# Kernel optimization log

Hardware: AMD Instinct MI355X
Metric: run time of the kernel (lower is better)

Reference implementation:

```python
import jax, jax.numpy as jnp
import numpy as np

DIM = 512
NUM_HEADS = 8
HEAD_DIM = DIM // NUM_HEADS
FFN_DIM = 4 * DIM
EPS = 1e-6


def rmsnorm(x, w):
    rms = jnp.sqrt(jnp.mean(x * x, axis=-1, keepdims=True) + EPS)
    return x / rms * w


def setup_inputs() -> dict:
    key = jax.random.key(0)
    ks = jax.random.split(key, 8)
    B, T = 4, 2048
    x = jax.random.normal(ks[0], (B, T, DIM), dtype=jnp.float32)
    # Linear weights stored as [in, out] (transpose of torch layout)
    w_qkv = jax.random.normal(ks[1], (DIM, 3 * DIM), dtype=jnp.float32) * 0.02
    w_out = jax.random.normal(ks[2], (DIM, DIM), dtype=jnp.float32) * 0.02
    b_out = jnp.zeros((DIM,), dtype=jnp.float32)
    w1 = jax.random.normal(ks[3], (DIM, FFN_DIM), dtype=jnp.float32) * 0.02
    b1 = jnp.zeros((FFN_DIM,), dtype=jnp.float32)
    w2 = jax.random.normal(ks[4], (FFN_DIM, DIM), dtype=jnp.float32) * 0.02
    b2 = jnp.zeros((DIM,), dtype=jnp.float32)
    norm1_w = jnp.ones((DIM,), dtype=jnp.float32)
    norm2_w = jnp.ones((DIM,), dtype=jnp.float32)
    return {
        "x": x, "norm1_w": norm1_w, "norm2_w": norm2_w,
        "w_qkv": w_qkv, "w_out": w_out, "b_out": b_out,
        "w1": w1, "b1": b1, "w2": w2, "b2": b2,
        "context_size": 64,
    }


def reference(x, norm1_w, norm2_w, w_qkv, w_out, b_out, w1, b1, w2, b2, context_size):
    B, T, D = x.shape
    H, Hd = NUM_HEADS, HEAD_DIM
    # --- attention sublayer ---
    xn = rmsnorm(x, norm1_w)
    qkv = xn @ w_qkv                      # (B, T, 3D)
    q, k, v = jnp.split(qkv, 3, axis=-1)
    q = q.reshape(B, T, H, Hd).transpose(0, 2, 1, 3)  # (B, H, T, Hd)
    k = k.reshape(B, T, H, Hd).transpose(0, 2, 1, 3)
    v = v.reshape(B, T, H, Hd).transpose(0, 2, 1, 3)
    scale = Hd ** -0.5
    scores = jnp.einsum('bhqd,bhkd->bhqk', q, k) * scale  # (B, H, T, T)
    idx = jnp.arange(T)
    band = jnp.abs(idx[:, None] - idx[None, :]) <= context_size  # (T, T)
    scores = jnp.where(band[None, None], scores, -jnp.inf)
    attn = jax.nn.softmax(scores, axis=-1)
    out = jnp.einsum('bhqk,bhkd->bhqd', attn, v)  # (B, H, T, Hd)
    out = out.transpose(0, 2, 1, 3).reshape(B, T, D)
    out = out @ w_out + b_out
    x = x + out
    # --- FFN sublayer ---
    h = rmsnorm(x, norm2_w)
    h = jax.nn.gelu(h @ w1 + b1, approximate=False)
    x = x + (h @ w2 + b2)
    return x
```

## Files before the change

kernel.cpp:

```cpp
#include <hip/hip_runtime.h>
#include <cstdint>
#include <cstddef>

#define B_  4
#define T_  2048
#define D_  512
#define NH_ 8
#define HD_ 64
#define FF_ 2048
#define M_  (B_*T_)

typedef unsigned short u16;
typedef __attribute__((ext_vector_type(8))) unsigned short u16x8;
typedef __attribute__((ext_vector_type(8))) __bf16         bf16x8;
typedef __attribute__((ext_vector_type(4))) float          f32x4;

__device__ __forceinline__ u16 f2bf(float f) {
  unsigned u = __float_as_uint(f);
  u += 0x7FFF + ((u >> 16) & 1);
  return (u16)(u >> 16);
}

__device__ __forceinline__ f32x4 mfma_bf16(u16x8 a, u16x8 b, f32x4 c) {
  return __builtin_amdgcn_mfma_f32_16x16x32_bf16(
      __builtin_bit_cast(bf16x8, a), __builtin_bit_cast(bf16x8, b), c, 0, 0, 0);
}

__device__ __forceinline__ void async16(const void* g, void* l) {
  __builtin_amdgcn_global_load_lds(
      (const __attribute__((address_space(1))) unsigned int*)g,
      (__attribute__((address_space(3))) unsigned int*)l, 16, 0, 0);
}

__global__ __launch_bounds__(256) void trans_kernel(const float* __restrict__ in,
                                                    u16* __restrict__ out,
                                                    int R, int C) {
  __shared__ float tile[32][33];
  int c0 = blockIdx.x * 32, r0 = blockIdx.y * 32;
  int tx = threadIdx.x, ty = threadIdx.y;
#pragma unroll
  for (int i = 0; i < 4; i++)
    tile[ty + i * 8][tx] = in[(size_t)(r0 + ty + i * 8) * C + c0 + tx];
  __syncthreads();
#pragma unroll
  for (int i = 0; i < 4; i++)
    out[(size_t)(c0 + ty + i * 8) * R + r0 + tx] = f2bf(tile[tx][ty + i * 8]);
}

__global__ __launch_bounds__(256) void rmsnorm_kernel(const float* __restrict__ x,
                                                      const float* __restrict__ w,
                                                      u16* __restrict__ out) {
  int row  = blockIdx.x * 4 + (threadIdx.x >> 6);
  int lane = threadIdx.x & 63;
  const float* xr = x + (size_t)row * D_ + lane * 8;
  float4 v0 = *(const float4*)xr;
  float4 v1 = *(const float4*)(xr + 4);
  float ss = v0.x*v0.x + v0.y*v0.y + v0.z*v0.z + v0.w*v0.w
           + v1.x*v1.x + v1.y*v1.y + v1.z*v1.z + v1.w*v1.w;
#pragma unroll
  for (int m = 1; m < 64; m <<= 1) ss += __shfl_xor(ss, m, 64);
  float inv = rsqrtf(ss * (1.0f / D_) + 1e-6f);
  const float* wr = w + lane * 8;
  float4 w0 = *(const float4*)wr;
  float4 w1v = *(const float4*)(wr + 4);
  u16 o[8];
  o[0] = f2bf(v0.x * inv * w0.x);  o[1] = f2bf(v0.y * inv * w0.y);
  o[2] = f2bf(v0.z * inv * w0.z);  o[3] = f2bf(v0.w * inv * w0.w);
  o[4] = f2bf(v1.x * inv * w1v.x); o[5] = f2bf(v1.y * inv * w1v.y);
  o[6] = f2bf(v1.z * inv * w1v.z); o[7] = f2bf(v1.w * inv * w1v.w);
  *(uint4*)(out + (size_t)row * D_ + lane * 8) = *(uint4*)o;
}

template <int BN, bool HAS_BIAS, bool HAS_RES, bool DO_GELU, bool STORE_BF16>
__global__ __launch_bounds__(256) void gemm_kernel(
    const u16* __restrict__ A, const u16* __restrict__ Bt, void* __restrict__ Cv,
    const float* __restrict__ bias, const float* __restrict__ res,
    int M, int N, int K) {
  constexpr int BCH = BN / 32;
  constexpr int NJ  = BN / 32;
  constexpr int EW  = BN + 4;
  __shared__ __align__(16) char smem[16384 + BN * 128];
  u16* ldsA = (u16*)smem;
  u16* ldsB = (u16*)(smem + 16384);
  const int tid = threadIdx.x;
  const int lane = tid & 63, w = tid >> 6;
  const int quad = lane >> 4, m16 = lane & 15;
  const int wm = w & 1, wn = w >> 1;
  const int m0 = blockIdx.y * 128, n0 = blockIdx.x * BN;

  f32x4 acc[4][NJ];
#pragma unroll
  for (int i = 0; i < 4; i++)
#pragma unroll
    for (int j = 0; j < NJ; j++) acc[i][j] = (f32x4){0.f, 0.f, 0.f, 0.f};

  const int srow = tid >> 3;
  const int scol = (((tid & 7) ^ (srow & 7))) * 8;
  const u16* Ag = A  + (size_t)(m0 + srow) * K + scol;
  const u16* Bg = Bt + (size_t)(n0 + srow) * K + scol;

  for (int kt = 0; kt < K; kt += 64) {
#pragma unroll
    for (int c = 0; c < 4; c++)
      async16(Ag + (size_t)c * 32 * K + kt, smem + c * 4096 + tid * 16);
#pragma unroll
    for (int c = 0; c < BCH; c++)
      async16(Bg + (size_t)c * 32 * K + kt, smem + 16384 + c * 4096 + tid * 16);
    __syncthreads();
#pragma unroll
    for (int kk = 0; kk < 2; kk++) {
      const int sl = ((kk * 4 + quad) ^ (m16 & 7)) * 8;
      const u16* pa = ldsA + (wm * 64 + m16) * 64 + sl;
      const u16* pb = ldsB + (wn * (BN / 2) + m16) * 64 + sl;
      u16x8 af[4], bfr[NJ];
#pragma unroll
      for (int i = 0; i < 4; i++) af[i] = *(const u16x8*)(pa + i * 1024);
#pragma unroll
      for (int j = 0; j < NJ; j++) bfr[j] = *(const u16x8*)(pb + j * 1024);
#pragma unroll
      for (int i = 0; i < 4; i++)
#pragma unroll
        for (int j = 0; j < NJ; j++)
          acc[i][j] = mfma_bf16(af[i], bfr[j], acc[i][j]);
    }
    __syncthreads();
  }

  float* eps = (float*)smem;
#pragma unroll
  for (int i = 0; i < 4; i++) {
    __syncthreads();
#pragma unroll
    for (int j = 0; j < NJ; j++)
#pragma unroll
      for (int r = 0; r < 4; r++)
        eps[(wm * 16 + quad * 4 + r) * EW + wn * (BN / 2) + j * 16 + m16] =
            acc[i][j][r];
    __syncthreads();
    constexpr int REPS = (32 * BN) / (256 * 8);
#pragma unroll
    for (int rep = 0; rep < REPS; rep++) {
      const int lr  = (BN == 128) ? (rep * 16 + (tid >> 4)) : (tid >> 3);
      const int col = (BN == 128) ? ((tid & 15) * 8) : ((tid & 7) * 8);
      const int rg  = m0 + (lr >> 4) * 64 + i * 16 + (lr & 15);
      float v[8];
      *(float4*)(v)     = *(const float4*)(eps + lr * EW + col);
      *(float4*)(v + 4) = *(const float4*)(eps + lr * EW + col + 4);
      if (HAS_BIAS) {
        float4 b0 = *(const float4*)(bias + n0 + col);
        float4 b1 = *(const float4*)(bias + n0 + col + 4);
        v[0] += b0.x; v[1] += b0.y; v[2] += b0.z; v[3] += b0.w;
        v[4] += b1.x; v[5] += b1.y; v[6] += b1.z; v[7] += b1.w;
      }
      if (DO_GELU) {
#pragma unroll
        for (int e = 0; e < 8; e++)
          v[e] = 0.5f * v[e] * (1.0f + erff(v[e] * 0.70710678118f));
      }
      const size_t idx = (size_t)rg * N + n0 + col;
      if (HAS_RES) {
        float4 r0 = *(const float4*)(res + idx);
        float4 r1 = *(const float4*)(res + idx + 4);
        v[0] += r0.x; v[1] += r0.y; v[2] += r0.z; v[3] += r0.w;
        v[4] += r1.x; v[5] += r1.y; v[6] += r1.z; v[7] += r1.w;
      }
      if (STORE_BF16) {
        u16 o[8];
#pragma unroll
        for (int e = 0; e < 8; e++) o[e] = f2bf(v[e]);
        *(uint4*)((u16*)Cv + idx) = *(uint4*)o;
      } else {
        *(float4*)((float*)Cv + idx)     = *(float4*)(v);
        *(float4*)((float*)Cv + idx + 4) = *(float4*)(v + 4);
      }
    }
  }
}

#define KP_ 72
__global__ __launch_bounds__(256) void attn_kernel(const u16* __restrict__ qkv,
                                                   u16* __restrict__ out) {
  __shared__ __align__(16) char smem[57600];
  u16* Ks = (u16*)smem;
  u16* Vt = (u16*)(smem + 29952);
  const int tid = threadIdx.x, lane = tid & 63, w = tid >> 6;
  const int quad = lane >> 4, m16 = lane & 15;
  const int q0 = blockIdx.x * 64, h = blockIdx.y, b = blockIdx.z;
  const int kstart = q0 - 64;
  const u16* base = qkv + (size_t)b * T_ * 1536;

  for (int c = tid; c < 1664; c += 256) {
    int row = c >> 3, cc = (c & 7) * 8;
    int j = kstart + row;
    j = j < 0 ? 0 : (j > T_ - 1 ? T_ - 1 : j);
    *(uint4*)(Ks + row * KP_ + cc) =
        *(const uint4*)(base + (size_t)j * 1536 + 512 + h * 64 + cc);
  }
  for (int c = tid; c < 1664; c += 256) {
    int row = c >> 3, cc = (c & 7) * 8;
    int j = kstart + row;
    j = j < 0 ? 0 : (j > T_ - 1 ? T_ - 1 : j);
    uint4 u = *(const uint4*)(base + (size_t)j * 1536 + 1024 + h * 64 + cc);
    u16 tmp[8];
    *(uint4*)tmp = u;
#pragma unroll
    for (int i = 0; i < 8; i++) Vt[(cc + i) * 216 + row] = tmp[i];
  }
  const int qw = q0 + w * 16;
  const u16* qb = base + (size_t)(qw + m16) * 1536 + h * 64 + quad * 8;
  u16x8 a0 = *(const u16x8*)qb;
  u16x8 a1 = *(const u16x8*)(qb + 32);
  __syncthreads();

  float s[10][4];
#pragma unroll
  for (int t = 0; t < 10; t++) {
    int kt = (w + t) * 16;
    u16x8 kb0 = *(const u16x8*)(Ks + (kt + m16) * KP_ + quad * 8);
    u16x8 kb1 = *(const u16x8*)(Ks + (kt + m16) * KP_ + 32 + quad * 8);
    f32x4 acc = {0.f, 0.f, 0.f, 0.f};
    acc = mfma_bf16(a0, kb0, acc);
    acc = mfma_bf16(a1, kb1, acc);
    int jab = kstart + kt + m16;
#pragma unroll
    for (int r = 0; r < 4; r++) {
      int q = qw + quad * 4 + r;
      int d = q - jab;
      bool valid = (jab >= 0) && (jab < T_) && (d <= 64) && (d >= -64);
      s[t][r] = valid ? acc[r] * 0.125f : -1e30f;
    }
  }
  float mx[4], sm[4];
#pragma unroll
  for (int r = 0; r < 4; r++) mx[r] = -1e30f;
#pragma unroll
  for (int t = 0; t < 10; t++)
#pragma unroll
    for (int r = 0; r < 4; r++) mx[r] = fmaxf(mx[r], s[t][r]);
#pragma unroll
  for (int r = 0; r < 4; r++) {
#pragma unroll
    for (int msk = 1; msk < 16; msk <<= 1)
      mx[r] = fmaxf(mx[r], __shfl_xor(mx[r], msk, 64));
    sm[r] = 0.f;
  }
#pragma unroll
  for (int t = 0; t < 10; t++)
#pragma unroll
    for (int r = 0; r < 4; r++) {
      float e = __expf(s[t][r] - mx[r]);
      s[t][r] = e; sm[r] += e;
    }
#pragma unroll
  for (int r = 0; r < 4; r++) {
#pragma unroll
    for (int msk = 1; msk < 16; msk <<= 1) sm[r] += __shfl_xor(sm[r], msk, 64);
    sm[r] = 1.0f / sm[r];
  }
  __syncthreads();
  u16* Ps = (u16*)smem + w * 2688;
#pragma unroll
  for (int t = 0; t < 10; t++)
#pragma unroll
    for (int r = 0; r < 4; r++)
      Ps[(quad * 4 + r) * 168 + t * 16 + m16] = f2bf(s[t][r] * sm[r]);
  __syncthreads();

  f32x4 o[4];
#pragma unroll
  for (int dt = 0; dt < 4; dt++) o[dt] = (f32x4){0.f, 0.f, 0.f, 0.f};
#pragma unroll
  for (int c5 = 0; c5 < 5; c5++) {
    u16x8 pa = *(const u16x8*)(Ps + m16 * 168 + c5 * 32 + quad * 8);
#pragma unroll
    for (int dt = 0; dt < 4; dt++) {
      u16x8 vb = *(const u16x8*)(Vt + (dt * 16 + m16) * 216 + w * 16 + c5 * 32 + quad * 8);
      o[dt] = mfma_bf16(pa, vb, o[dt]);
    }
  }
#pragma unroll
  for (int dt = 0; dt < 4; dt++)
#pragma unroll
    for (int r = 0; r < 4; r++)
      out[(size_t)(b * T_ + qw + quad * 4 + r) * D_ + h * HD_ + dt * 16 + m16] =
          f2bf(o[dt][r]);
}

extern "C" void kernel_launch(void* const* d_in, const int* in_sizes, int n_in,
                              void* d_out, int out_size, void* d_ws, size_t ws_size,
                              hipStream_t stream) {
  (void)in_sizes; (void)n_in; (void)out_size; (void)ws_size;
  const float* x     = (const float*)d_in[0];
  const float* n1w   = (const float*)d_in[1];
  const float* n2w   = (const float*)d_in[2];
  const float* w_qkv = (const float*)d_in[3];
  const float* w_out = (const float*)d_in[4];
  const float* b_out = (const float*)d_in[5];
  const float* w1    = (const float*)d_in[6];
  const float* b1    = (const float*)d_in[7];
  const float* w2    = (const float*)d_in[8];
  const float* b2    = (const float*)d_in[9];
  float* out = (float*)d_out;
  char* ws = (char*)d_ws;

  u16* wqkvT  = (u16*)(ws + 0);
  u16* woutT  = (u16*)(ws + 1572864);
  u16* w1T    = (u16*)(ws + 2097152);
  u16* w2T    = (u16*)(ws + 4194304);
  u16* xn     = (u16*)(ws + 6291456);
  u16* qkv    = (u16*)(ws + 14680064);
  u16* attno  = (u16*)(ws + 39845888);
  float* x1   = (float*)(ws + 48234496);
  u16* hn     = xn;
  u16* hbuf   = qkv;

  dim3 tb(32, 8);
  trans_kernel<<<dim3(48, 16), tb, 0, stream>>>(w_qkv, wqkvT, 512, 1536);
  trans_kernel<<<dim3(16, 16), tb, 0, stream>>>(w_out, woutT, 512, 512);
  trans_kernel<<<dim3(64, 16), tb, 0, stream>>>(w1,   w1T,   512, 2048);
  trans_kernel<<<dim3(16, 64), tb, 0, stream>>>(w2,   w2T,   2048, 512);

  rmsnorm_kernel<<<2048, 256, 0, stream>>>(x, n1w, xn);
  gemm_kernel<128, false, false, false, true><<<dim3(12, 64), 256, 0, stream>>>(
      xn, wqkvT, (void*)qkv, nullptr, nullptr, M_, 3 * D_, D_);
  attn_kernel<<<dim3(32, 8, 4), 256, 0, stream>>>(qkv, attno);
  gemm_kernel<64, true, true, false, false><<<dim3(8, 64), 256, 0, stream>>>(
      attno, woutT, (void*)x1, b_out, x, M_, D_, D_);
  rmsnorm_kernel<<<2048, 256, 0, stream>>>(x1, n2w, hn);
  gemm_kernel<128, true, false, true, true><<<dim3(16, 64), 256, 0, stream>>>(
      hn, w1T, (void*)hbuf, b1, nullptr, M_, FF_, D_);
  gemm_kernel<64, true, true, false, false><<<dim3(8, 64), 256, 0, stream>>>(
      hbuf, w2T, (void*)out, b2, x1, M_, D_, FF_);
}
```

Baseline: 244.8 us.

## Merge weight transposes, add BM tiling, fast GELU, pad V tile

Fuses the four weight-transpose launches into one kernel, and makes the GEMM block-M size a template parameter so the N=512 GEMMs run 64x64 tiles over twice as many blocks. It also hoists the bias loads out of the epilogue loop and replaces erff in GELU with an Abramowitz-Stegun polynomial using a fast reciprocal and exp. Separately, it changes the transposed-V LDS row pitch from 216 to 218 to reduce bank conflicts. The GELU approximation has roughly 1e-7 absolute error and may use an approximate reciprocal.

```diff
diff --git a/kernel.cpp b/kernel.cpp
--- a/kernel.cpp
+++ b/kernel.cpp
@@ -32,11 +32,34 @@
       (__attribute__((address_space(3))) unsigned int*)l, 16, 0, 0);
 }
 
-__global__ __launch_bounds__(256) void trans_kernel(const float* __restrict__ in,
-                                                    u16* __restrict__ out,
-                                                    int R, int C) {
+__device__ __forceinline__ float gelu_f(float v) {
+  float ax = fabsf(v) * 0.70710678118f;
+#if __has_builtin(__builtin_amdgcn_rcpf)
+  float t = __builtin_amdgcn_rcpf(1.0f + 0.3275911f * ax);
+#else
+  float t = 1.0f / (1.0f + 0.3275911f * ax);
+#endif
+  float p = ((((1.061405429f * t - 1.453152027f) * t + 1.421413741f) * t
+              - 0.284496736f) * t + 0.254829592f) * t;
+  float e = __expf(-ax * ax);
+  float er = 1.0f - p * e;
+  float s = (v >= 0.0f) ? er : -er;
+  return 0.5f * v * (1.0f + s);
+}
+
+__global__ __launch_bounds__(256) void trans4_kernel(
+    const float* __restrict__ i0, u16* __restrict__ o0,
+    const float* __restrict__ i1, u16* __restrict__ o1,
+    const float* __restrict__ i2, u16* __restrict__ o2,
+    const float* __restrict__ i3, u16* __restrict__ o3) {
   __shared__ float tile[32][33];
-  int c0 = blockIdx.x * 32, r0 = blockIdx.y * 32;
+  int bid = blockIdx.x;
+  const float* in; u16* out; int R, C, gx, lb;
+  if (bid < 768)       { in = i0; out = o0; R = 512;  C = 1536; gx = 48; lb = bid; }
+  else if (bid < 1024) { in = i1; out = o1; R = 512;  C = 512;  gx = 16; lb = bid - 768; }
+  else if (bid < 2048) { in = i2; out = o2; R = 512;  C = 2048; gx = 64; lb = bid - 1024; }
+  else                 { in = i3; out = o3; R = 2048; C = 512;  gx = 16; lb = bid - 2048; }
+  int c0 = (lb % gx) * 32, r0 = (lb / gx) * 32;
   int tx = threadIdx.x, ty = threadIdx.y;
 #pragma unroll
   for (int i = 0; i < 4; i++)
@@ -71,26 +94,28 @@
   *(uint4*)(out + (size_t)row * D_ + lane * 8) = *(uint4*)o;
 }
 
-template <int BN, bool HAS_BIAS, bool HAS_RES, bool DO_GELU, bool STORE_BF16>
+template <int BM, int BN, bool HAS_BIAS, bool HAS_RES, bool DO_GELU, bool STORE_BF16>
 __global__ __launch_bounds__(256) void gemm_kernel(
     const u16* __restrict__ A, const u16* __restrict__ Bt, void* __restrict__ Cv,
     const float* __restrict__ bias, const float* __restrict__ res,
     int M, int N, int K) {
+  constexpr int ACH = BM / 32;
   constexpr int BCH = BN / 32;
-  constexpr int NJ  = BN / 32;
+  constexpr int WM  = BM / 2, WN = BN / 2;
+  constexpr int MI  = WM / 16, NJ = WN / 16;
   constexpr int EW  = BN + 4;
-  __shared__ __align__(16) char smem[16384 + BN * 128];
+  __shared__ __align__(16) char smem[BM * 128 + BN * 128];
   u16* ldsA = (u16*)smem;
-  u16* ldsB = (u16*)(smem + 16384);
+  u16* ldsB = (u16*)(smem + BM * 128);
   const int tid = threadIdx.x;
   const int lane = tid & 63, w = tid >> 6;
   const int quad = lane >> 4, m16 = lane & 15;
   const int wm = w & 1, wn = w >> 1;
-  const int m0 = blockIdx.y * 128, n0 = blockIdx.x * BN;
-
-  f32x4 acc[4][NJ];
-#pragma unroll
-  for (int i = 0; i < 4; i++)
+  const int m0 = blockIdx.y * BM, n0 = blockIdx.x * BN;
+
+  f32x4 acc[MI][NJ];
+#pragma unroll
+  for (int i = 0; i < MI; i++)
 #pragma unroll
     for (int j = 0; j < NJ; j++) acc[i][j] = (f32x4){0.f, 0.f, 0.f, 0.f};
 
@@ -101,24 +126,24 @@
 
   for (int kt = 0; kt < K; kt += 64) {
 #pragma unroll
-    for (int c = 0; c < 4; c++)
+    for (int c = 0; c < ACH; c++)
       async16(Ag + (size_t)c * 32 * K + kt, smem + c * 4096 + tid * 16);
 #pragma unroll
     for (int c = 0; c < BCH; c++)
-      async16(Bg + (size_t)c * 32 * K + kt, smem + 16384 + c * 4096 + tid * 16);
+      async16(Bg + (size_t)c * 32 * K + kt, smem + BM * 128 + c * 4096 + tid * 16);
     __syncthreads();
 #pragma unroll
     for (int kk = 0; kk < 2; kk++) {
       const int sl = ((kk * 4 + quad) ^ (m16 & 7)) * 8;
-      const u16* pa = ldsA + (wm * 64 + m16) * 64 + sl;
-      const u16* pb = ldsB + (wn * (BN / 2) + m16) * 64 + sl;
-      u16x8 af[4], bfr[NJ];
-#pragma unroll
-      for (int i = 0; i < 4; i++) af[i] = *(const u16x8*)(pa + i * 1024);
+      const u16* pa = ldsA + (wm * WM + m16) * 64 + sl;
+      const u16* pb = ldsB + (wn * WN + m16) * 64 + sl;
+      u16x8 af[MI], bfr[NJ];
+#pragma unroll
+      for (int i = 0; i < MI; i++) af[i] = *(const u16x8*)(pa + i * 1024);
 #pragma unroll
       for (int j = 0; j < NJ; j++) bfr[j] = *(const u16x8*)(pb + j * 1024);
 #pragma unroll
-      for (int i = 0; i < 4; i++)
+      for (int i = 0; i < MI; i++)
 #pragma unroll
         for (int j = 0; j < NJ; j++)
           acc[i][j] = mfma_bf16(af[i], bfr[j], acc[i][j]);
@@ -127,35 +152,41 @@
   }
 
   float* eps = (float*)smem;
-#pragma unroll
-  for (int i = 0; i < 4; i++) {
+  constexpr int REPS = (32 * BN) / (256 * 8);
+  float bv[REPS][8];
+  if (HAS_BIAS) {
+#pragma unroll
+    for (int rep = 0; rep < REPS; rep++) {
+      const int col = (BN == 128) ? ((tid & 15) * 8) : ((tid & 7) * 8);
+      *(float4*)(bv[rep])     = *(const float4*)(bias + n0 + col);
+      *(float4*)(bv[rep] + 4) = *(const float4*)(bias + n0 + col + 4);
+    }
+  }
+#pragma unroll
+  for (int i = 0; i < MI; i++) {
     __syncthreads();
 #pragma unroll
     for (int j = 0; j < NJ; j++)
 #pragma unroll
       for (int r = 0; r < 4; r++)
-        eps[(wm * 16 + quad * 4 + r) * EW + wn * (BN / 2) + j * 16 + m16] =
+        eps[(wm * 16 + quad * 4 + r) * EW + wn * WN + j * 16 + m16] =
             acc[i][j][r];
     __syncthreads();
-    constexpr int REPS = (32 * BN) / (256 * 8);
 #pragma unroll
     for (int rep = 0; rep < REPS; rep++) {
       const int lr  = (BN == 128) ? (rep * 16 + (tid >> 4)) : (tid >> 3);
       const int col = (BN == 128) ? ((tid & 15) * 8) : ((tid & 7) * 8);
-      const int rg  = m0 + (lr >> 4) * 64 + i * 16 + (lr & 15);
+      const int rg  = m0 + (lr >> 4) * WM + i * 16 + (lr & 15);
       float v[8];
       *(float4*)(v)     = *(const float4*)(eps + lr * EW + col);
       *(float4*)(v + 4) = *(const float4*)(eps + lr * EW + col + 4);
       if (HAS_BIAS) {
-        float4 b0 = *(const float4*)(bias + n0 + col);
-        float4 b1 = *(const float4*)(bias + n0 + col + 4);
-        v[0] += b0.x; v[1] += b0.y; v[2] += b0.z; v[3] += b0.w;
-        v[4] += b1.x; v[5] += b1.y; v[6] += b1.z; v[7] += b1.w;
+#pragma unroll
+        for (int e = 0; e < 8; e++) v[e] += bv[rep][e];
       }
       if (DO_GELU) {
 #pragma unroll
-        for (int e = 0; e < 8; e++)
-          v[e] = 0.5f * v[e] * (1.0f + erff(v[e] * 0.70710678118f));
+        for (int e = 0; e < 8; e++) v[e] = gelu_f(v[e]);
       }
       const size_t idx = (size_t)rg * N + n0 + col;
       if (HAS_RES) {
@@ -178,9 +209,10 @@
 }
 
 #define KP_ 72
+#define VP_ 218
 __global__ __launch_bounds__(256) void attn_kernel(const u16* __restrict__ qkv,
                                                    u16* __restrict__ out) {
-  __shared__ __align__(16) char smem[57600];
+  __shared__ __align__(16) char smem[29952 + 64 * VP_ * 2];
   u16* Ks = (u16*)smem;
   u16* Vt = (u16*)(smem + 29952);
   const int tid = threadIdx.x, lane = tid & 63, w = tid >> 6;
@@ -204,7 +236,7 @@
     u16 tmp[8];
     *(uint4*)tmp = u;
 #pragma unroll
-    for (int i = 0; i < 8; i++) Vt[(cc + i) * 216 + row] = tmp[i];
+    for (int i = 0; i < 8; i++) Vt[(cc + i) * VP_ + row] = tmp[i];
   }
   const int qw = q0 + w * 16;
   const u16* qb = base + (size_t)(qw + m16) * 1536 + h * 64 + quad * 8;
@@ -274,7 +306,7 @@
     u16x8 pa = *(const u16x8*)(Ps + m16 * 168 + c5 * 32 + quad * 8);
 #pragma unroll
     for (int dt = 0; dt < 4; dt++) {
-      u16x8 vb = *(const u16x8*)(Vt + (dt * 16 + m16) * 216 + w * 16 + c5 * 32 + quad * 8);
+      u16x8 vb = *(const u16x8*)(Vt + (dt * 16 + m16) * VP_ + w * 16 + c5 * 32 + quad * 8);
       o[dt] = mfma_bf16(pa, vb, o[dt]);
     }
   }
@@ -314,21 +346,18 @@
   u16* hn     = xn;
   u16* hbuf   = qkv;
 
-  dim3 tb(32, 8);
-  trans_kernel<<<dim3(48, 16), tb, 0, stream>>>(w_qkv, wqkvT, 512, 1536);
-  trans_kernel<<<dim3(16, 16), tb, 0, stream>>>(w_out, woutT, 512, 512);
-  trans_kernel<<<dim3(64, 16), tb, 0, stream>>>(w1,   w1T,   512, 2048);
-  trans_kernel<<<dim3(16, 64), tb, 0, stream>>>(w2,   w2T,   2048, 512);
+  trans4_kernel<<<3072, dim3(32, 8), 0, stream>>>(
+      w_qkv, wqkvT, w_out, woutT, w1, w1T, w2, w2T);
 
   rmsnorm_kernel<<<2048, 256, 0, stream>>>(x, n1w, xn);
-  gemm_kernel<128, false, false, false, true><<<dim3(12, 64), 256, 0, stream>>>(
+  gemm_kernel<128, 128, false, false, false, true><<<dim3(12, 64), 256, 0, stream>>>(
       xn, wqkvT, (void*)qkv, nullptr, nullptr, M_, 3 * D_, D_);
   attn_kernel<<<dim3(32, 8, 4), 256, 0, stream>>>(qkv, attno);
-  gemm_kernel<64, true, true, false, false><<<dim3(8, 64), 256, 0, stream>>>(
+  gemm_kernel<64, 64, true, true, false, false><<<dim3(8, 128), 256, 0, stream>>>(
       attno, woutT, (void*)x1, b_out, x, M_, D_, D_);
   rmsnorm_kernel<<<2048, 256, 0, stream>>>(x1, n2w, hn);
-  gemm_kernel<128, true, false, true, true><<<dim3(16, 64), 256, 0, stream>>>(
+  gemm_kernel<128, 128, true, false, true, true><<<dim3(16, 64), 256, 0, stream>>>(
       hn, w1T, (void*)hbuf, b1, nullptr, M_, FF_, D_);
-  gemm_kernel<64, true, true, false, false><<<dim3(8, 64), 256, 0, stream>>>(
+  gemm_kernel<64, 64, true, true, false, false><<<dim3(8, 128), 256, 0, stream>>>(
       hbuf, w2T, (void*)out, b2, x1, M_, D_, FF_);
 }
```

Measured after the change: 246.0 us. About the same (+0.5%).
